# Kernel optimization log

Measured on AMD Instinct MI355X. Metric: run time of the kernel, lower is better.

The kernel has to match this reference:

```python
import jax, jax.numpy as jnp
import numpy as np

E = 8
HID = 2048
INTER = 1408
TOT = 8192


def setup_inputs() -> dict:
    key = jax.random.key(0)
    k1, k2, k3, k4, k5 = jax.random.split(key, 5)
    # uneven token counts per expert that sum exactly to TOT (grouped-GEMM ragged sizes)
    deltas = np.array([512, -256, 128, -384, 256, -512, 384, -128], dtype=np.int32)
    tokens_per_expert = jnp.asarray(TOT // E + deltas, dtype=jnp.int32)  # sums to TOT
    permuted_x = jax.random.normal(k1, (TOT, HID), dtype=jnp.float32)
    permuted_probs = jax.random.uniform(k2, (TOT,), dtype=jnp.float32)
    s_in = 1.0 / np.sqrt(HID)
    s_mid = 1.0 / np.sqrt(INTER)
    w_gate = jax.random.normal(k3, (E, HID, INTER), dtype=jnp.float32) * s_in
    w_up = jax.random.normal(k4, (E, HID, INTER), dtype=jnp.float32) * s_in
    w_down = jax.random.normal(k5, (E, INTER, HID), dtype=jnp.float32) * s_mid
    return {
        "permuted_x": permuted_x,
        "permuted_probs": permuted_probs,
        "w_gate": w_gate,
        "w_up": w_up,
        "w_down": w_down,
        "tokens_per_expert": tokens_per_expert,
    }


def reference(permuted_x, permuted_probs, w_gate, w_up, w_down, tokens_per_expert):
    # Grouped GEMM: tokens sorted by expert; lax.ragged_dot contracts each
    # contiguous group of rows against its expert's weight without padding.
    gate = jax.lax.ragged_dot(permuted_x, w_gate, tokens_per_expert)  # [T, INTER]
    up = jax.lax.ragged_dot(permuted_x, w_up, tokens_per_expert)      # [T, INTER]
    h = jax.nn.silu(gate) * up                                         # fused SiLU-mul
    values = jax.lax.ragged_dot(h, w_down, tokens_per_expert)          # [T, HID]
    return permuted_probs[:, None].astype(values.dtype) * values
```

## Files before the change

kernel.cpp:

```cpp
#include <hip/hip_runtime.h>

typedef unsigned short u16;
typedef unsigned int u32;
typedef u16 us8 __attribute__((ext_vector_type(8)));
typedef __bf16 bf16x8 __attribute__((ext_vector_type(8)));
typedef float f32x4 __attribute__((ext_vector_type(4)));

constexpr int kE = 8;
constexpr int kHID = 2048;
constexpr int kINTER = 1408;
constexpr int kTOT = 8192;

static __device__ __forceinline__ u16 f2bf(float f) {
  u32 u = __float_as_uint(f);
  u32 r = (u + 0x7fffu + ((u >> 16) & 1u)) >> 16;
  return (u16)r;
}

static __device__ __forceinline__ void gll16(const u16* g, u16* l) {
  __builtin_amdgcn_global_load_lds(
      (const __attribute__((address_space(1))) u32*)g,
      (__attribute__((address_space(3))) u32*)l, 16, 0, 0);
}

__global__ void conv_bf16(const float* __restrict__ x, u16* __restrict__ o) {
  size_t i = ((size_t)blockIdx.x * 256 + threadIdx.x) * 8;
  const float4* p = (const float4*)(x + i);
  float4 f0 = p[0], f1 = p[1];
  us8 v;
  v[0] = f2bf(f0.x); v[1] = f2bf(f0.y); v[2] = f2bf(f0.z); v[3] = f2bf(f0.w);
  v[4] = f2bf(f1.x); v[5] = f2bf(f1.y); v[6] = f2bf(f1.z); v[7] = f2bf(f1.w);
  *(us8*)(o + i) = v;
}

__global__ void transp_bf16(const float* __restrict__ w, u16* __restrict__ wt,
                            int K, int N) {
  __shared__ float tile[64][65];
  int e = blockIdx.z;
  const float* we = w + (size_t)e * K * N;
  u16* wte = wt + (size_t)e * K * N;
  int n0 = blockIdx.x * 64, k0 = blockIdx.y * 64;
  int t = threadIdx.x;
  int kl = t >> 4, n4 = (t & 15) * 4;
#pragma unroll
  for (int r = 0; r < 4; r++) {
    int k = r * 16 + kl;
    float4 v = *(const float4*)(we + (size_t)(k0 + k) * N + n0 + n4);
    tile[k][n4 + 0] = v.x; tile[k][n4 + 1] = v.y;
    tile[k][n4 + 2] = v.z; tile[k][n4 + 3] = v.w;
  }
  __syncthreads();
#pragma unroll
  for (int r = 0; r < 2; r++) {
    int c = r * 256 + t;
    int n = c >> 3, kc = (c & 7) * 8;
    us8 o;
#pragma unroll
    for (int j = 0; j < 8; j++) o[j] = f2bf(tile[kc + j][n]);
    *(us8*)(wte + (size_t)(n0 + n) * K + k0 + kc) = o;
  }
}

static __device__ __forceinline__ bool expert_of_tile256(
    const int* __restrict__ tpe, int ty, int& e, int& m0, int& m_end) {
  int tile_base = 0, row_base = 0;
  e = -1;
  for (int i = 0; i < kE; i++) {
    int tc = tpe[i];
    int nt = (tc + 255) >> 8;
    if (e < 0 && ty < tile_base + nt) {
      e = i;
      m0 = row_base + (ty - tile_base) * 256;
      m_end = row_base + tc;
    }
    tile_base += nt;
    row_base += tc;
  }
  return e >= 0;
}

static __device__ __forceinline__ void map_block(int& bx, int& by) {
  int nx = gridDim.x, ny = gridDim.y;
  int nwg = nx * ny;
  int flat = blockIdx.y * nx + blockIdx.x;
  int q = nwg >> 3, r = nwg & 7;
  int xcd = flat & 7, lid = flat >> 3;
  int nf = (xcd < r ? xcd * (q + 1) : r * (q + 1) + (xcd - r) * q) + lid;
  const int G = 4;
  int gs = G * nx;
  int grp = nf / gs;
  int wi = nf - grp * gs;
  int rows = ny - grp * G;
  if (rows > G) rows = G;
  bx = wi / rows;
  by = grp * G + (wi - bx * rows);
}

__launch_bounds__(512, 2)
__global__ void gemm1(const u16* __restrict__ Xb, const u16* __restrict__ Wgt,
                      const u16* __restrict__ Wut, const float* __restrict__ probs,
                      const int* __restrict__ tpe, u16* __restrict__ H) {
  __shared__ __align__(16) u16 sm[65536];
  u16* A0 = sm;           u16* A1 = sm + 16384;
  u16* Bg0 = sm + 32768;  u16* Bg1 = sm + 40960;
  u16* Bu0 = sm + 49152;  u16* Bu1 = sm + 57344;

  int bx, by; map_block(bx, by);
  int e, m0, m_end;
  if (!expert_of_tile256(tpe, by, e, m0, m_end)) return;
  int n0 = bx * 128;

  int t = threadIdx.x;
  int w = t >> 6, lane = t & 63;
  int quad = lane >> 4, l15 = lane & 15;
  int wm = (w >> 1) * 64, wn = (w & 1) * 64;

  int trow = t >> 3;
  int cg = (t & 7) ^ (trow & 7);
  const u16* gA[4];
#pragma unroll
  for (int rr = 0; rr < 4; rr++) {
    int row = m0 + rr * 64 + trow;
    if (row > kTOT - 1) row = kTOT - 1;
    gA[rr] = Xb + (size_t)row * kHID + cg * 8;
  }
  const u16 *gBg[2], *gBu[2];
#pragma unroll
  for (int rr = 0; rr < 2; rr++) {
    size_t nrow = (size_t)e * kINTER + n0 + rr * 64 + trow;
    gBg[rr] = Wgt + nrow * kHID + cg * 8;
    gBu[rr] = Wut + nrow * kHID + cg * 8;
  }

  int abase = (wm + l15) * 64;
  int bbase = (wn + l15) * 64;
  int sz0 = ((quad ^ (l15 & 7)) << 3);
  int sz1 = (((4 | quad) ^ (l15 & 7)) << 3);

  f32x4 accg[4][4] = {};
  f32x4 accu[4][4] = {};

  auto stage = [&](u16* A, u16* Bg, u16* Bu, int ko) {
#pragma unroll
    for (int rr = 0; rr < 4; rr++) gll16(gA[rr] + ko, A + (rr * 64 + w * 8) * 64);
#pragma unroll
    for (int rr = 0; rr < 2; rr++) {
      gll16(gBg[rr] + ko, Bg + (rr * 64 + w * 8) * 64);
      gll16(gBu[rr] + ko, Bu + (rr * 64 + w * 8) * 64);
    }
  };
  auto compute = [&](const u16* A, const u16* Bg, const u16* Bu) {
#pragma unroll
    for (int ks = 0; ks < 2; ks++) {
      int sz = ks ? sz1 : sz0;
      bf16x8 a[4], bg[4], bu[4];
#pragma unroll
      for (int i = 0; i < 4; i++) a[i] = *(const bf16x8*)(A + abase + i * 1024 + sz);
#pragma unroll
      for (int j = 0; j < 4; j++) {
        bg[j] = *(const bf16x8*)(Bg + bbase + j * 1024 + sz);
        bu[j] = *(const bf16x8*)(Bu + bbase + j * 1024 + sz);
      }
#pragma unroll
      for (int i = 0; i < 4; i++)
#pragma unroll
        for (int j = 0; j < 4; j++) {
          accg[i][j] = __builtin_amdgcn_mfma_f32_16x16x32_bf16(a[i], bg[j], accg[i][j], 0, 0, 0);
          accu[i][j] = __builtin_amdgcn_mfma_f32_16x16x32_bf16(a[i], bu[j], accu[i][j], 0, 0, 0);
        }
    }
  };

  stage(A0, Bg0, Bu0, 0);
  __syncthreads();
  for (int kt = 0; kt < kHID / 64; kt += 2) {
    stage(A1, Bg1, Bu1, (kt + 1) * 64);
    compute(A0, Bg0, Bu0);
    __syncthreads();
    if (kt + 2 < kHID / 64) stage(A0, Bg0, Bu0, (kt + 2) * 64);
    compute(A1, Bg1, Bu1);
    __syncthreads();
  }

#pragma unroll
  for (int i = 0; i < 4; i++) {
#pragma unroll
    for (int r = 0; r < 4; r++) {
      int row = m0 + wm + i * 16 + quad * 4 + r;
      if (row < m_end) {
        float p = probs[row];
#pragma unroll
        for (int j = 0; j < 4; j++) {
          int col = n0 + wn + j * 16 + l15;
          float g = accg[i][j][r], u = accu[i][j][r];
          float s = g / (1.0f + __expf(-g));
          H[(size_t)row * kINTER + col] = f2bf(s * u * p);
        }
      }
    }
  }
}

__launch_bounds__(512, 2)
__global__ void gemm2(const u16* __restrict__ H, const u16* __restrict__ Wdt,
                      const int* __restrict__ tpe, float* __restrict__ out) {
  __shared__ __align__(16) u16 sm[65536];
  u16* A0 = sm;          u16* A1 = sm + 16384;
  u16* B0 = sm + 32768;  u16* B1 = sm + 49152;

  int bx, by; map_block(bx, by);
  int e, m0, m_end;
  if (!expert_of_tile256(tpe, by, e, m0, m_end)) return;
  int n0 = bx * 256;

  int t = threadIdx.x;
  int w = t >> 6, lane = t & 63;
  int quad = lane >> 4, l15 = lane & 15;
  int wm = (w >> 2) * 128, wn = (w & 3) * 64;

  int trow = t >> 3;
  int cg = (t & 7) ^ (trow & 7);
  const u16* gA[4];
#pragma unroll
  for (int rr = 0; rr < 4; rr++) {
    int row = m0 + rr * 64 + trow;
    if (row > kTOT - 1) row = kTOT - 1;
    gA[rr] = H + (size_t)row * kINTER + cg * 8;
  }
  const u16* gB[4];
#pragma unroll
  for (int rr = 0; rr < 4; rr++) {
    size_t nrow = (size_t)e * kHID + n0 + rr * 64 + trow;
    gB[rr] = Wdt + nrow * kINTER + cg * 8;
  }

  int abase = (wm + l15) * 64;
  int bbase = (wn + l15) * 64;
  int sz0 = ((quad ^ (l15 & 7)) << 3);
  int sz1 = (((4 | quad) ^ (l15 & 7)) << 3);

  f32x4 acc[8][4] = {};

  auto stage = [&](u16* A, u16* B, int ko) {
#pragma unroll
    for (int rr = 0; rr < 4; rr++) gll16(gA[rr] + ko, A + (rr * 64 + w * 8) * 64);
#pragma unroll
    for (int rr = 0; rr < 4; rr++) gll16(gB[rr] + ko, B + (rr * 64 + w * 8) * 64);
  };
  auto compute = [&](const u16* A, const u16* B) {
#pragma unroll
    for (int ks = 0; ks < 2; ks++) {
      int sz = ks ? sz1 : sz0;
      bf16x8 a[8], b[4];
#pragma unroll
      for (int i = 0; i < 8; i++) a[i] = *(const bf16x8*)(A + abase + i * 1024 + sz);
#pragma unroll
      for (int j = 0; j < 4; j++) b[j] = *(const bf16x8*)(B + bbase + j * 1024 + sz);
#pragma unroll
      for (int i = 0; i < 8; i++)
#pragma unroll
        for (int j = 0; j < 4; j++)
          acc[i][j] = __builtin_amdgcn_mfma_f32_16x16x32_bf16(a[i], b[j], acc[i][j], 0, 0, 0);
    }
  };

  stage(A0, B0, 0);
  __syncthreads();
  for (int kt = 0; kt < kINTER / 64; kt += 2) {
    stage(A1, B1, (kt + 1) * 64);
    compute(A0, B0);
    __syncthreads();
    if (kt + 2 < kINTER / 64) stage(A0, B0, (kt + 2) * 64);
    compute(A1, B1);
    __syncthreads();
  }

#pragma unroll
  for (int i = 0; i < 8; i++) {
#pragma unroll
    for (int r = 0; r < 4; r++) {
      int row = m0 + wm + i * 16 + quad * 4 + r;
      if (row < m_end) {
#pragma unroll
        for (int j = 0; j < 4; j++) {
          int col = n0 + wn + j * 16 + l15;
          out[(size_t)row * kHID + col] = acc[i][j][r];
        }
      }
    }
  }
}

extern "C" void kernel_launch(void* const* d_in, const int* in_sizes, int n_in,
                              void* d_out, int out_size, void* d_ws, size_t ws_size,
                              hipStream_t stream) {
  const float* x = (const float*)d_in[0];
  const float* probs = (const float*)d_in[1];
  const float* wg = (const float*)d_in[2];
  const float* wu = (const float*)d_in[3];
  const float* wd = (const float*)d_in[4];
  const int* tpe = (const int*)d_in[5];
  float* out = (float*)d_out;

  u16* ws = (u16*)d_ws;
  u16* Xb = ws;
  u16* Wgt = Xb + (size_t)kTOT * kHID;
  u16* Wut = Wgt + (size_t)kE * kINTER * kHID;
  u16* Wdt = Wut + (size_t)kE * kINTER * kHID;
  u16* H = Wdt + (size_t)kE * kHID * kINTER;

  conv_bf16<<<(kTOT * kHID) / (256 * 8), 256, 0, stream>>>(x, Xb);
  transp_bf16<<<dim3(kINTER / 64, kHID / 64, kE), 256, 0, stream>>>(wg, Wgt, kHID, kINTER);
  transp_bf16<<<dim3(kINTER / 64, kHID / 64, kE), 256, 0, stream>>>(wu, Wut, kHID, kINTER);
  transp_bf16<<<dim3(kHID / 64, kINTER / 64, kE), 256, 0, stream>>>(wd, Wdt, kINTER, kHID);

  gemm1<<<dim3(kINTER / 128, 39), 512, 0, stream>>>(Xb, Wgt, Wut, probs, tpe, H);
  gemm2<<<dim3(kHID / 256, 39), 512, 0, stream>>>(H, Wdt, tpe, out);
}
```

Measured before the change: 535.5 us.

## Drop weight transpose kernels; read untransposed B via ds_read_b64_tr_b16

Replaces the three weight transpose-and-convert kernels with plain fp32-to-bf16 conversion that keeps the original K-major layout. The GEMMs now stage B tiles row-major in LDS and build MFMA fragments with the LDS transpose-read instruction, removing the costly strided transpose pass. gemm2 also moves to 256x128 tiles with a smaller accumulator and less LDS, which doubles its block count. Risks include explicit lgkmcnt waits that serialize LDS reads before MFMAs, and possible bank conflicts in the new B layout.

```diff
diff --git a/kernel.cpp b/kernel.cpp
--- a/kernel.cpp
+++ b/kernel.cpp
@@ -5,6 +5,8 @@
 typedef u16 us8 __attribute__((ext_vector_type(8)));
 typedef __bf16 bf16x8 __attribute__((ext_vector_type(8)));
 typedef float f32x4 __attribute__((ext_vector_type(4)));
+typedef u32 u32x2 __attribute__((ext_vector_type(2)));
+typedef u32 u32x4 __attribute__((ext_vector_type(4)));
 
 constexpr int kE = 8;
 constexpr int kHID = 2048;
@@ -21,6 +23,23 @@
   __builtin_amdgcn_global_load_lds(
       (const __attribute__((address_space(1))) u32*)g,
       (__attribute__((address_space(3))) u32*)l, 16, 0, 0);
+}
+
+static __device__ __forceinline__ u32 lds_off(u16* p) {
+  return (u32)(uintptr_t)(__attribute__((address_space(3))) u16*)p;
+}
+
+template <int OFF>
+static __device__ __forceinline__ u32x2 trr(u32 va) {
+  u32x2 d;
+  asm volatile("ds_read_b64_tr_b16 %0, %1 offset:%2"
+               : "=v"(d) : "v"(va), "i"(OFF));
+  return d;
+}
+
+static __device__ __forceinline__ bf16x8 mkfrag(u32x2 lo, u32x2 hi) {
+  u32x4 c = {lo[0], lo[1], hi[0], hi[1]};
+  return __builtin_bit_cast(bf16x8, c);
 }
 
 __global__ void conv_bf16(const float* __restrict__ x, u16* __restrict__ o) {
@@ -31,34 +50,6 @@
   v[0] = f2bf(f0.x); v[1] = f2bf(f0.y); v[2] = f2bf(f0.z); v[3] = f2bf(f0.w);
   v[4] = f2bf(f1.x); v[5] = f2bf(f1.y); v[6] = f2bf(f1.z); v[7] = f2bf(f1.w);
   *(us8*)(o + i) = v;
-}
-
-__global__ void transp_bf16(const float* __restrict__ w, u16* __restrict__ wt,
-                            int K, int N) {
-  __shared__ float tile[64][65];
-  int e = blockIdx.z;
-  const float* we = w + (size_t)e * K * N;
-  u16* wte = wt + (size_t)e * K * N;
-  int n0 = blockIdx.x * 64, k0 = blockIdx.y * 64;
-  int t = threadIdx.x;
-  int kl = t >> 4, n4 = (t & 15) * 4;
-#pragma unroll
-  for (int r = 0; r < 4; r++) {
-    int k = r * 16 + kl;
-    float4 v = *(const float4*)(we + (size_t)(k0 + k) * N + n0 + n4);
-    tile[k][n4 + 0] = v.x; tile[k][n4 + 1] = v.y;
-    tile[k][n4 + 2] = v.z; tile[k][n4 + 3] = v.w;
-  }
-  __syncthreads();
-#pragma unroll
-  for (int r = 0; r < 2; r++) {
-    int c = r * 256 + t;
-    int n = c >> 3, kc = (c & 7) * 8;
-    us8 o;
-#pragma unroll
-    for (int j = 0; j < 8; j++) o[j] = f2bf(tile[kc + j][n]);
-    *(us8*)(wte + (size_t)(n0 + n) * K + k0 + kc) = o;
-  }
 }
 
 static __device__ __forceinline__ bool expert_of_tile256(
@@ -97,13 +88,10 @@
 }
 
 __launch_bounds__(512, 2)
-__global__ void gemm1(const u16* __restrict__ Xb, const u16* __restrict__ Wgt,
-                      const u16* __restrict__ Wut, const float* __restrict__ probs,
+__global__ void gemm1(const u16* __restrict__ Xb, const u16* __restrict__ Wgb,
+                      const u16* __restrict__ Wub, const float* __restrict__ probs,
                       const int* __restrict__ tpe, u16* __restrict__ H) {
   __shared__ __align__(16) u16 sm[65536];
-  u16* A0 = sm;           u16* A1 = sm + 16384;
-  u16* Bg0 = sm + 32768;  u16* Bg1 = sm + 40960;
-  u16* Bu0 = sm + 49152;  u16* Bu1 = sm + 57344;
 
   int bx, by; map_block(bx, by);
   int e, m0, m_end;
@@ -124,42 +112,65 @@
     if (row > kTOT - 1) row = kTOT - 1;
     gA[rr] = Xb + (size_t)row * kHID + cg * 8;
   }
-  const u16 *gBg[2], *gBu[2];
-#pragma unroll
-  for (int rr = 0; rr < 2; rr++) {
-    size_t nrow = (size_t)e * kINTER + n0 + rr * 64 + trow;
-    gBg[rr] = Wgt + nrow * kHID + cg * 8;
-    gBu[rr] = Wut + nrow * kHID + cg * 8;
-  }
+
+  int q = lane & 7;
+  int s0 = w * 16 + (lane >> 3);
+  int kb0 = s0 >> 3, nb0 = s0 & 7;
+  size_t wbase = (size_t)e * kHID * kINTER;
+  const u16* gBg = Wgb + wbase + (size_t)(kb0 * 4 + (q >> 1)) * kINTER
+                   + n0 + nb0 * 16 + (q & 1) * 8;
+  const u16* gBu = Wub + wbase + (size_t)(kb0 * 4 + (q >> 1)) * kINTER
+                   + n0 + nb0 * 16 + (q & 1) * 8;
 
   int abase = (wm + l15) * 64;
-  int bbase = (wn + l15) * 64;
   int sz0 = ((quad ^ (l15 & 7)) << 3);
   int sz1 = (((4 | quad) ^ (l15 & 7)) << 3);
 
+  u32 smb = lds_off(sm);
+  u32 bgoff = quad * 2048 + (w & 1) * 512 + l15 * 8;
+
   f32x4 accg[4][4] = {};
   f32x4 accu[4][4] = {};
 
-  auto stage = [&](u16* A, u16* Bg, u16* Bu, int ko) {
-#pragma unroll
-    for (int rr = 0; rr < 4; rr++) gll16(gA[rr] + ko, A + (rr * 64 + w * 8) * 64);
-#pragma unroll
-    for (int rr = 0; rr < 2; rr++) {
-      gll16(gBg[rr] + ko, Bg + (rr * 64 + w * 8) * 64);
-      gll16(gBu[rr] + ko, Bu + (rr * 64 + w * 8) * 64);
-    }
+  auto stage = [&](int buf, int kt) {
+    u16* Ab = sm + buf * 16384;
+#pragma unroll
+    for (int rr = 0; rr < 4; rr++)
+      gll16(gA[rr] + (size_t)kt * 64, Ab + (rr * 64 + w * 8) * 64);
+    u16* Bg = sm + 32768 + buf * 8192;
+    u16* Bu = sm + 49152 + buf * 8192;
+    const u16* pg = gBg + (size_t)kt * 64 * kINTER;
+    const u16* pu = gBu + (size_t)kt * 64 * kINTER;
+    gll16(pg, Bg + w * 1024);
+    gll16(pg + (size_t)4 * kINTER, Bg + w * 1024 + 512);
+    gll16(pu, Bu + w * 1024);
+    gll16(pu + (size_t)4 * kINTER, Bu + w * 1024 + 512);
   };
-  auto compute = [&](const u16* A, const u16* Bg, const u16* Bu) {
+  auto compute = [&](int buf) {
+    const u16* A = sm + buf * 16384;
+    u32 bg_base = smb + 65536 + buf * 16384 + bgoff;
+    u32 bu_base = bg_base + 32768;
 #pragma unroll
     for (int ks = 0; ks < 2; ks++) {
       int sz = ks ? sz1 : sz0;
-      bf16x8 a[4], bg[4], bu[4];
+      bf16x8 a[4];
 #pragma unroll
       for (int i = 0; i < 4; i++) a[i] = *(const bf16x8*)(A + abase + i * 1024 + sz);
+      u32x2 rg[4][2], ru[4][2];
 #pragma unroll
       for (int j = 0; j < 4; j++) {
-        bg[j] = *(const bf16x8*)(Bg + bbase + j * 1024 + sz);
-        bu[j] = *(const bf16x8*)(Bu + bbase + j * 1024 + sz);
+        u32 vg = bg_base + ks * 8192 + j * 128;
+        rg[j][0] = trr<0>(vg); rg[j][1] = trr<1024>(vg);
+        u32 vu = bu_base + ks * 8192 + j * 128;
+        ru[j][0] = trr<0>(vu); ru[j][1] = trr<1024>(vu);
+      }
+      asm volatile("s_waitcnt lgkmcnt(0)" ::: "memory");
+      __builtin_amdgcn_sched_barrier(0);
+      bf16x8 bg[4], bu[4];
+#pragma unroll
+      for (int j = 0; j < 4; j++) {
+        bg[j] = mkfrag(rg[j][0], rg[j][1]);
+        bu[j] = mkfrag(ru[j][0], ru[j][1]);
       }
 #pragma unroll
       for (int i = 0; i < 4; i++)
@@ -171,14 +182,15 @@
     }
   };
 
-  stage(A0, Bg0, Bu0, 0);
+  constexpr int NK = kHID / 64;
+  stage(0, 0);
   __syncthreads();
-  for (int kt = 0; kt < kHID / 64; kt += 2) {
-    stage(A1, Bg1, Bu1, (kt + 1) * 64);
-    compute(A0, Bg0, Bu0);
+  for (int kt = 0; kt < NK; kt += 2) {
+    stage(1, kt + 1);
+    compute(0);
     __syncthreads();
-    if (kt + 2 < kHID / 64) stage(A0, Bg0, Bu0, (kt + 2) * 64);
-    compute(A1, Bg1, Bu1);
+    if (kt + 2 < NK) stage(0, kt + 2);
+    compute(1);
     __syncthreads();
   }
 
@@ -202,21 +214,19 @@
 }
 
 __launch_bounds__(512, 2)
-__global__ void gemm2(const u16* __restrict__ H, const u16* __restrict__ Wdt,
+__global__ void gemm2(const u16* __restrict__ H, const u16* __restrict__ Wdb,
                       const int* __restrict__ tpe, float* __restrict__ out) {
-  __shared__ __align__(16) u16 sm[65536];
-  u16* A0 = sm;          u16* A1 = sm + 16384;
-  u16* B0 = sm + 32768;  u16* B1 = sm + 49152;
+  __shared__ __align__(16) u16 sm[49152];
 
   int bx, by; map_block(bx, by);
   int e, m0, m_end;
   if (!expert_of_tile256(tpe, by, e, m0, m_end)) return;
-  int n0 = bx * 256;
+  int n0 = bx * 128;
 
   int t = threadIdx.x;
   int w = t >> 6, lane = t & 63;
   int quad = lane >> 4, l15 = lane & 15;
-  int wm = (w >> 2) * 128, wn = (w & 3) * 64;
+  int wm = (w >> 1) * 64, wn = (w & 1) * 64;
 
   int trow = t >> 3;
   int cg = (t & 7) ^ (trow & 7);
@@ -227,56 +237,75 @@
     if (row > kTOT - 1) row = kTOT - 1;
     gA[rr] = H + (size_t)row * kINTER + cg * 8;
   }
-  const u16* gB[4];
-#pragma unroll
-  for (int rr = 0; rr < 4; rr++) {
-    size_t nrow = (size_t)e * kHID + n0 + rr * 64 + trow;
-    gB[rr] = Wdt + nrow * kINTER + cg * 8;
-  }
+
+  int q = lane & 7;
+  int s0 = w * 16 + (lane >> 3);
+  int kb0 = s0 >> 3, nb0 = s0 & 7;
+  const u16* gB = Wdb + (size_t)e * kINTER * kHID
+                  + (size_t)(kb0 * 4 + (q >> 1)) * kHID
+                  + n0 + nb0 * 16 + (q & 1) * 8;
 
   int abase = (wm + l15) * 64;
-  int bbase = (wn + l15) * 64;
   int sz0 = ((quad ^ (l15 & 7)) << 3);
   int sz1 = (((4 | quad) ^ (l15 & 7)) << 3);
 
-  f32x4 acc[8][4] = {};
-
-  auto stage = [&](u16* A, u16* B, int ko) {
-#pragma unroll
-    for (int rr = 0; rr < 4; rr++) gll16(gA[rr] + ko, A + (rr * 64 + w * 8) * 64);
-#pragma unroll
-    for (int rr = 0; rr < 4; rr++) gll16(gB[rr] + ko, B + (rr * 64 + w * 8) * 64);
+  u32 smb = lds_off(sm);
+  u32 boff = quad * 2048 + (w & 1) * 512 + l15 * 8;
+
+  f32x4 acc[4][4] = {};
+
+  auto stage = [&](int buf, int kt) {
+    u16* Ab = sm + buf * 16384;
+#pragma unroll
+    for (int rr = 0; rr < 4; rr++)
+      gll16(gA[rr] + (size_t)kt * 64, Ab + (rr * 64 + w * 8) * 64);
+    u16* B = sm + 32768 + buf * 8192;
+    const u16* pb = gB + (size_t)kt * 64 * kHID;
+    gll16(pb, B + w * 1024);
+    gll16(pb + (size_t)4 * kHID, B + w * 1024 + 512);
   };
-  auto compute = [&](const u16* A, const u16* B) {
+  auto compute = [&](int buf) {
+    const u16* A = sm + buf * 16384;
+    u32 b_base = smb + 65536 + buf * 16384 + boff;
 #pragma unroll
     for (int ks = 0; ks < 2; ks++) {
       int sz = ks ? sz1 : sz0;
-      bf16x8 a[8], b[4];
-#pragma unroll
-      for (int i = 0; i < 8; i++) a[i] = *(const bf16x8*)(A + abase + i * 1024 + sz);
-#pragma unroll
-      for (int j = 0; j < 4; j++) b[j] = *(const bf16x8*)(B + bbase + j * 1024 + sz);
-#pragma unroll
-      for (int i = 0; i < 8; i++)
+      bf16x8 a[4];
+#pragma unroll
+      for (int i = 0; i < 4; i++) a[i] = *(const bf16x8*)(A + abase + i * 1024 + sz);
+      u32x2 rb[4][2];
+#pragma unroll
+      for (int j = 0; j < 4; j++) {
+        u32 vb = b_base + ks * 8192 + j * 128;
+        rb[j][0] = trr<0>(vb); rb[j][1] = trr<1024>(vb);
+      }
+      asm volatile("s_waitcnt lgkmcnt(0)" ::: "memory");
+      __builtin_amdgcn_sched_barrier(0);
+      bf16x8 b[4];
+#pragma unroll
+      for (int j = 0; j < 4; j++) b[j] = mkfrag(rb[j][0], rb[j][1]);
+#pragma unroll
+      for (int i = 0; i < 4; i++)
 #pragma unroll
         for (int j = 0; j < 4; j++)
           acc[i][j] = __builtin_amdgcn_mfma_f32_16x16x32_bf16(a[i], b[j], acc[i][j], 0, 0, 0);
     }
   };
 
-  stage(A0, B0, 0);
+  constexpr int NK = kINTER / 64;
+  stage(0, 0);
   __syncthreads();
-  for (int kt = 0; kt < kINTER / 64; kt += 2) {
-    stage(A1, B1, (kt + 1) * 64);
-    compute(A0, B0);
+  for (int kt = 0; kt < NK; kt += 2) {
+    stage(1, kt + 1);
+    compute(0);
     __syncthreads();
-    if (kt + 2 < kINTER / 64) stage(A0, B0, (kt + 2) * 64);
-    compute(A1, B1);
+    if (kt + 2 < NK) stage(0, kt + 2);
+    compute(1);
     __syncthreads();
   }
 
 #pragma unroll
-  for (int i = 0; i < 8; i++) {
+  for (int i = 0; i < 4; i++) {
 #pragma unroll
     for (int r = 0; r < 4; r++) {
       int row = m0 + wm + i * 16 + quad * 4 + r;
@@ -304,16 +333,17 @@
 
   u16* ws = (u16*)d_ws;
   u16* Xb = ws;
-  u16* Wgt = Xb + (size_t)kTOT * kHID;
-  u16* Wut = Wgt + (size_t)kE * kINTER * kHID;
-  u16* Wdt = Wut + (size_t)kE * kINTER * kHID;
-  u16* H = Wdt + (size_t)kE * kHID * kINTER;
-
-  conv_bf16<<<(kTOT * kHID) / (256 * 8), 256, 0, stream>>>(x, Xb);
-  transp_bf16<<<dim3(kINTER / 64, kHID / 64, kE), 256, 0, stream>>>(wg, Wgt, kHID, kINTER);
-  transp_bf16<<<dim3(kINTER / 64, kHID / 64, kE), 256, 0, stream>>>(wu, Wut, kHID, kINTER);
-  transp_bf16<<<dim3(kHID / 64, kINTER / 64, kE), 256, 0, stream>>>(wd, Wdt, kINTER, kHID);
-
-  gemm1<<<dim3(kINTER / 128, 39), 512, 0, stream>>>(Xb, Wgt, Wut, probs, tpe, H);
-  gemm2<<<dim3(kHID / 256, 39), 512, 0, stream>>>(H, Wdt, tpe, out);
-}
+  u16* Wgb = Xb + (size_t)kTOT * kHID;
+  u16* Wub = Wgb + (size_t)kE * kHID * kINTER;
+  u16* Wdb = Wub + (size_t)kE * kHID * kINTER;
+  u16* H = Wdb + (size_t)kE * kINTER * kHID;
+
+  constexpr int kWE = kE * kHID * kINTER;
+  conv_bf16<<<(kTOT * kHID) / 2048, 256, 0, stream>>>(x, Xb);
+  conv_bf16<<<kWE / 2048, 256, 0, stream>>>(wg, Wgb);
+  conv_bf16<<<kWE / 2048, 256, 0, stream>>>(wu, Wub);
+  conv_bf16<<<kWE / 2048, 256, 0, stream>>>(wd, Wdb);
+
+  gemm1<<<dim3(kINTER / 128, 39), 512, 0, stream>>>(Xb, Wgb, Wub, probs, tpe, H);
+  gemm2<<<dim3(kHID / 128, 39), 512, 0, stream>>>(H, Wdb, tpe, out);
+}
```

Measured after the change: 690.0 us. 28.8% more time.
